# Optimization experiments

Hardware: AMD Instinct MI355X
Metric: run time of the kernel (lower is better)

The kernel has to match this reference:

```python
import jax, jax.numpy as jnp
import numpy as np

R_SAFE = 0.8

def setup_inputs() -> dict:
    key = jax.random.key(0)
    ks = jax.random.split(key, 12)
    B, F, H1, H21, H22, C = 524288, 10, 128, 32, 32, 2
    def lin(k, fan_in, fan_out):
        k1, k2 = jax.random.split(k)
        bound = 1.0 / np.sqrt(fan_in)
        W = jax.random.uniform(k1, (fan_out, fan_in), jnp.float32, -bound, bound)
        b = jax.random.uniform(k2, (fan_out,), jnp.float32, -bound, bound)
        return W, b
    W1, b1 = lin(ks[0], F, H1)
    W21, b21 = lin(ks[1], H1, H21)
    W22, b22 = lin(ks[2], H1, H22)
    W31, b31 = lin(ks[3], H21, C)
    W32, b32 = lin(ks[4], H22, 1)
    obs = jax.random.normal(ks[5], (B, F), jnp.float32)
    return {"obs": obs, "W1": W1, "b1": b1, "W21": W21, "b21": b21,
            "W22": W22, "b22": b22, "W31": W31, "b31": b31, "W32": W32, "b32": b32}

def _forward(obs, W1, b1, W21, b21, W22, b22, W31, b31, W32, b32):
    x = jax.nn.silu(obs @ W1.T + b1)          # [B, H1]
    x21 = jax.nn.silu(x @ W21.T + b21)        # [B, H21]
    x22 = jax.nn.silu(x @ W22.T + b22)        # [B, H22]
    unom = x21 @ W31.T + b31                  # [B, 2]
    alpha = 4.0 * jax.nn.sigmoid((x22 @ W32.T + b32)[:, 0])  # [B]
    rel_x, rel_y = obs[:, 6], obs[:, 7]
    v_hx, v_hy = obs[:, 8], obs[:, 9]
    barrier = rel_x**2 + rel_y**2 - R_SAFE**2
    lf = -2.0 * (rel_x * v_hx + rel_y * v_hy)
    # single inequality G u <= h with G = [-2 rel_x, -2 rel_y]
    G = jnp.stack([-2.0 * rel_x, -2.0 * rel_y], axis=1)      # [B, 2]
    h = lf + alpha * barrier                                  # [B]
    # QP: min ||u - unom||^2 s.t. G u <= h  ->  halfspace projection (exact KKT)
    gg = jnp.sum(G * G, axis=1)                               # [B]
    viol = jnp.sum(G * unom, axis=1) - h                      # [B]
    lam = jnp.where(gg > 0, jax.nn.relu(viol) / jnp.maximum(gg, 1e-12), 0.0)
    return unom - lam[:, None] * G

def reference(obs, W1, b1, W21, b21, W22, b22, W31, b31, W32, b32):
    return _forward(obs, W1, b1, W21, b21, W22, b22, W31, b31, W32, b32)
```

## Files before the change

kernel.cpp:

```cpp
#include <hip/hip_runtime.h>


typedef _Float16 half8 __attribute__((ext_vector_type(8)));
typedef float floatx4 __attribute__((ext_vector_type(4)));

#define TPB 256
#define NW  4

#define WS_FRAG 0
#define WS_B2Q  26624
#define WS_END  26880

__device__ __forceinline__ float fast_sigmoid(float z) {
    return __builtin_amdgcn_rcpf(1.0f + __expf(-z));
}

__device__ __forceinline__ void silu_pair(float z0, float z1,
                                          _Float16* o0, _Float16* o1) {
    float e0 = __expf(fminf(-z0, 30.0f));
    float e1 = __expf(fminf(-z1, 30.0f));
    float d0 = 1.0f + e0, d1 = 1.0f + e1;
    float r  = __builtin_amdgcn_rcpf(d0 * d1);
    *o0 = (_Float16)(z0 * d1 * r);
    *o1 = (_Float16)(z1 * d0 * r);
}

__global__ __launch_bounds__(256) void prep_kernel(
    const float* __restrict__ W1,  const float* __restrict__ b1,
    const float* __restrict__ W21, const float* __restrict__ b21,
    const float* __restrict__ W22, const float* __restrict__ b22,
    const float* __restrict__ W31, const float* __restrict__ b31,
    const float* __restrict__ W32, const float* __restrict__ b32,
    unsigned char* __restrict__ ws)
{
    const int tid  = blockIdx.x * 256 + threadIdx.x;
    const int lane = tid & 63;
    const int m    = lane & 15;
    const int q    = lane >> 4;

    if (tid < 26 * 64) {
        const int f = tid >> 6;
        float v[8];
        if (f < 8) {
            const float* wr = W1 + (f * 16 + m) * 10;
            #pragma unroll
            for (int j = 0; j < 8; ++j) {
                const int k = q * 8 + j;
                v[j] = (k < 10) ? wr[k] : (k == 10 ? b1[f * 16 + m] : 0.0f);
            }
        } else if (f < 24) {
            const int f2 = f - 8, nt2 = f2 >> 2, kt = f2 & 3;
            const int n2 = nt2 * 16 + m;
            const float* wr = (n2 < 32) ? (W21 + n2 * 128)
                                        : (W22 + (n2 - 32) * 128);
            #pragma unroll
            for (int j = 0; j < 8; ++j) {
                const int H = (2 * kt + (j >> 2)) * 16 + q * 4 + (j & 3);
                v[j] = wr[H];
            }
        } else {
            const int kt3 = f - 24;
            #pragma unroll
            for (int j = 0; j < 8; ++j) {
                const int H3 = (2 * kt3 + (j >> 2)) * 16 + q * 4 + (j & 3);
                float x = 0.0f;
                if (m == 0)      x = (H3 < 32)  ? W31[H3]       : 0.0f;
                else if (m == 1) x = (H3 < 32)  ? W31[32 + H3]  : 0.0f;
                else if (m == 2) x = (H3 >= 32) ? W32[H3 - 32]  : 0.0f;
                v[j] = x;
            }
        }
        half8 h;
        #pragma unroll
        for (int j = 0; j < 8; ++j) h[j] = (_Float16)v[j];
        ((half8*)(ws + WS_FRAG))[tid] = h;
    }
    if (tid < 16) {
        const int nt2 = tid >> 2, qq = tid & 3;
        float4 v;
        float* vp = (float*)&v;
        #pragma unroll
        for (int r = 0; r < 4; ++r) {
            const int n2 = nt2 * 16 + qq * 4 + r;
            vp[r] = (n2 < 32) ? b21[n2] : b22[n2 - 32];
        }
        ((float4*)(ws + WS_B2Q))[tid] = v;
    }
}

__global__ __launch_bounds__(TPB, 4) void barriernet_kernel(
    const float* __restrict__ obs,
    const unsigned char* __restrict__ ws,
    const float* __restrict__ b31, const float* __restrict__ b32,
    float* __restrict__ out, int B)
{
    __shared__ __align__(16) unsigned char lds[WS_END];

    const int tid  = threadIdx.x;
    const int wave = tid >> 6;
    const int lane = tid & 63;
    const int m    = lane & 15;
    const int q    = lane >> 4;

    {
        const float4* src = (const float4*)ws;
        float4* dst = (float4*)lds;
        for (int i = tid; i < WS_END / 16; i += TPB) dst[i] = src[i];
    }
    __syncthreads();

    const half8*  wl   = ((const half8*)lds) + lane;
    const float4* b2qt = (const float4*)(lds + WS_B2Q);

    const float bu0 = b31[0], bu1 = b31[1], bz3 = b32[0];

    const int tiles = (B + 15) >> 4;
    const int tbase = (blockIdx.x * NW + wave) * 2;

    const float* orow[2];
    half8 xf[2];
    int lrow0[2];
    #pragma unroll
    for (int p = 0; p < 2; ++p) {
        int tile = tbase + p;
        if (tile >= tiles) tile = tiles - 1;
        int lr = (tile << 4) + m;
        if (lr >= B) lr = B - 1;
        lrow0[p] = lr;
        orow[p] = obs + (size_t)lr * 10;

        float g0=0,g1=0,g2=0,g3=0,g4=0,g5=0,g6=0,g7=0;
        if (q == 0) {
            float2 p0 = *(const float2*)(orow[p] + 0);
            float2 p1 = *(const float2*)(orow[p] + 2);
            float2 p2 = *(const float2*)(orow[p] + 4);
            float2 p3 = *(const float2*)(orow[p] + 6);
            g0=p0.x; g1=p0.y; g2=p1.x; g3=p1.y;
            g4=p2.x; g5=p2.y; g6=p3.x; g7=p3.y;
        } else if (q == 1) {
            float2 pp = *(const float2*)(orow[p] + 8);
            g0=pp.x; g1=pp.y;
            g2=1.0f;
        }
        xf[p][0]=(_Float16)g0; xf[p][1]=(_Float16)g1;
        xf[p][2]=(_Float16)g2; xf[p][3]=(_Float16)g3;
        xf[p][4]=(_Float16)g4; xf[p][5]=(_Float16)g5;
        xf[p][6]=(_Float16)g6; xf[p][7]=(_Float16)g7;
    }

    half8 b2f[2][4];
    #pragma unroll
    for (int kt = 0; kt < 4; ++kt) {
        half8 w1a = wl[(2 * kt) * 64];
        half8 w1b = wl[(2 * kt + 1) * 64];
        #pragma unroll
        for (int p = 0; p < 2; ++p) {
            const floatx4 zz = {0.0f, 0.0f, 0.0f, 0.0f};
            floatx4 a0 = __builtin_amdgcn_mfma_f32_16x16x32_f16(
                             w1a, xf[p], zz, 0, 0, 0);
            floatx4 a1 = __builtin_amdgcn_mfma_f32_16x16x32_f16(
                             w1b, xf[p], zz, 0, 0, 0);
            half8 bf;
            #pragma unroll
            for (int jj = 0; jj < 4; ++jj) {
                _Float16 o0, o1;
                silu_pair(a0[jj], a1[jj], &o0, &o1);
                bf[jj] = o0; bf[jj + 4] = o1;
            }
            b2f[p][kt] = bf;
        }
    }

    floatx4 acc2[2][4];
    #pragma unroll
    for (int nt2 = 0; nt2 < 4; ++nt2) {
        float4 bi = b2qt[nt2 * 4 + q];
        floatx4 zi = {bi.x, bi.y, bi.z, bi.w};
        acc2[0][nt2] = zi;
        acc2[1][nt2] = zi;
        #pragma unroll
        for (int kt = 0; kt < 4; ++kt) {
            half8 wfr = wl[(8 + nt2 * 4 + kt) * 64];
            acc2[0][nt2] = __builtin_amdgcn_mfma_f32_16x16x32_f16(
                               wfr, b2f[0][kt], acc2[0][nt2], 0, 0, 0);
            acc2[1][nt2] = __builtin_amdgcn_mfma_f32_16x16x32_f16(
                               wfr, b2f[1][kt], acc2[1][nt2], 0, 0, 0);
        }
    }

    half8 b3f[2][2];
    #pragma unroll
    for (int kt3 = 0; kt3 < 2; ++kt3) {
        #pragma unroll
        for (int p = 0; p < 2; ++p) {
            half8 bf;
            #pragma unroll
            for (int jj = 0; jj < 4; ++jj) {
                _Float16 o0, o1;
                silu_pair(acc2[p][2 * kt3][jj], acc2[p][2 * kt3 + 1][jj],
                          &o0, &o1);
                bf[jj] = o0; bf[jj + 4] = o1;
            }
            b3f[p][kt3] = bf;
        }
    }

    half8 w3a = wl[24 * 64];
    half8 w3b = wl[25 * 64];
    #pragma unroll
    for (int p = 0; p < 2; ++p) {
        floatx4 d = {0.0f, 0.0f, 0.0f, 0.0f};
        d = __builtin_amdgcn_mfma_f32_16x16x32_f16(w3a, b3f[p][0], d, 0, 0, 0);
        d = __builtin_amdgcn_mfma_f32_16x16x32_f16(w3b, b3f[p][1], d, 0, 0, 0);
        if (q == 0) {
            const float u0  = d[0] + bu0;
            const float u1  = d[1] + bu1;
            const float z32 = d[2] + bz3;
            const float alpha = 4.0f * fast_sigmoid(z32);

            const float2 rxy = *(const float2*)(orow[p] + 6);
            const float2 vxy = *(const float2*)(orow[p] + 8);
            const float rx = rxy.x, ry = rxy.y, vx = vxy.x, vy = vxy.y;

            const float barrier = rx * rx + ry * ry - 0.64f;
            const float lf = -2.0f * (rx * vx + ry * vy);
            const float gx = -2.0f * rx, gy = -2.0f * ry;
            const float h  = lf + alpha * barrier;
            const float gg = gx * gx + gy * gy;
            const float viol = gx * u0 + gy * u1 - h;
            float lam = 0.0f;
            if (gg > 0.0f)
                lam = fmaxf(viol, 0.0f) *
                      __builtin_amdgcn_rcpf(fmaxf(gg, 1e-12f));

            float2 r;
            r.x = fmaf(-lam, gx, u0);
            r.y = fmaf(-lam, gy, u1);
            *(float2*)(out + (size_t)lrow0[p] * 2) = r;
        }
    }
}

extern "C" void kernel_launch(void* const* d_in, const int* in_sizes, int n_in,
                              void* d_out, int out_size, void* d_ws, size_t ws_size,
                              hipStream_t stream) {
    const float* obs = (const float*)d_in[0];
    const float* W1  = (const float*)d_in[1];
    const float* b1  = (const float*)d_in[2];
    const float* W21 = (const float*)d_in[3];
    const float* b21 = (const float*)d_in[4];
    const float* W22 = (const float*)d_in[5];
    const float* b22 = (const float*)d_in[6];
    const float* W31 = (const float*)d_in[7];
    const float* b31 = (const float*)d_in[8];
    const float* W32 = (const float*)d_in[9];
    const float* b32 = (const float*)d_in[10];

    unsigned char* ws = (unsigned char*)d_ws;

    prep_kernel<<<7, 256, 0, stream>>>(W1, b1, W21, b21, W22, b22,
                                       W31, b31, W32, b32, ws);

    const int B = in_sizes[0] / 10;
    const int tiles = (B + 15) / 16;
    const int pairs = (tiles + 1) / 2;
    const int grid  = (pairs + NW - 1) / NW;

    barriernet_kernel<<<grid, TPB, 0, stream>>>(obs, ws, b31, b32,
                                                (float*)d_out, B);
}
```

Before: 115.4 us.

## Fuse weight prep into main kernel and fold log2e scaling into weights

Removes the separate prep kernel launch: every block now builds the fp16 MFMA weight fragments directly in LDS from the raw fp32 weights. The weights and biases are pre-scaled by log2(e), and the last layer by ln2, so SiLU can use exp2 with fewer multiplies and an FMA-based shared reciprocal. The obs rx/ry values are also reused from registers instead of being reloaded. The cost is that every block repeats the weight gather and conversion from global memory, and accuracy may shift slightly in fp16.

```diff
diff --git a/kernel.cpp b/kernel.cpp
--- a/kernel.cpp
+++ b/kernel.cpp
@@ -15,83 +15,24 @@
     return __builtin_amdgcn_rcpf(1.0f + __expf(-z));
 }
 
-__device__ __forceinline__ void silu_pair(float z0, float z1,
-                                          _Float16* o0, _Float16* o1) {
-    float e0 = __expf(fminf(-z0, 30.0f));
-    float e1 = __expf(fminf(-z1, 30.0f));
-    float d0 = 1.0f + e0, d1 = 1.0f + e1;
-    float r  = __builtin_amdgcn_rcpf(d0 * d1);
-    *o0 = (_Float16)(z0 * d1 * r);
-    *o1 = (_Float16)(z1 * d0 * r);
-}
-
-__global__ __launch_bounds__(256) void prep_kernel(
+__device__ __forceinline__ void silu2s(float y0, float y1,
+                                       _Float16* o0, _Float16* o1) {
+    float e0 = exp2f(-y0);
+    float e1 = exp2f(-y1);
+    float d1 = 1.0f + e1;
+    float P  = __builtin_fmaf(e0, d1, d1);
+    float r  = __builtin_amdgcn_rcpf(P);
+    *o0 = (_Float16)((y0 * d1) * r);
+    *o1 = (_Float16)(__builtin_fmaf(y1, e0, y1) * r);
+}
+
+__global__ __launch_bounds__(TPB, 4) void barriernet_kernel(
+    const float* __restrict__ obs,
     const float* __restrict__ W1,  const float* __restrict__ b1,
     const float* __restrict__ W21, const float* __restrict__ b21,
     const float* __restrict__ W22, const float* __restrict__ b22,
     const float* __restrict__ W31, const float* __restrict__ b31,
     const float* __restrict__ W32, const float* __restrict__ b32,
-    unsigned char* __restrict__ ws)
-{
-    const int tid  = blockIdx.x * 256 + threadIdx.x;
-    const int lane = tid & 63;
-    const int m    = lane & 15;
-    const int q    = lane >> 4;
-
-    if (tid < 26 * 64) {
-        const int f = tid >> 6;
-        float v[8];
-        if (f < 8) {
-            const float* wr = W1 + (f * 16 + m) * 10;
-            #pragma unroll
-            for (int j = 0; j < 8; ++j) {
-                const int k = q * 8 + j;
-                v[j] = (k < 10) ? wr[k] : (k == 10 ? b1[f * 16 + m] : 0.0f);
-            }
-        } else if (f < 24) {
-            const int f2 = f - 8, nt2 = f2 >> 2, kt = f2 & 3;
-            const int n2 = nt2 * 16 + m;
-            const float* wr = (n2 < 32) ? (W21 + n2 * 128)
-                                        : (W22 + (n2 - 32) * 128);
-            #pragma unroll
-            for (int j = 0; j < 8; ++j) {
-                const int H = (2 * kt + (j >> 2)) * 16 + q * 4 + (j & 3);
-                v[j] = wr[H];
-            }
-        } else {
-            const int kt3 = f - 24;
-            #pragma unroll
-            for (int j = 0; j < 8; ++j) {
-                const int H3 = (2 * kt3 + (j >> 2)) * 16 + q * 4 + (j & 3);
-                float x = 0.0f;
-                if (m == 0)      x = (H3 < 32)  ? W31[H3]       : 0.0f;
-                else if (m == 1) x = (H3 < 32)  ? W31[32 + H3]  : 0.0f;
-                else if (m == 2) x = (H3 >= 32) ? W32[H3 - 32]  : 0.0f;
-                v[j] = x;
-            }
-        }
-        half8 h;
-        #pragma unroll
-        for (int j = 0; j < 8; ++j) h[j] = (_Float16)v[j];
-        ((half8*)(ws + WS_FRAG))[tid] = h;
-    }
-    if (tid < 16) {
-        const int nt2 = tid >> 2, qq = tid & 3;
-        float4 v;
-        float* vp = (float*)&v;
-        #pragma unroll
-        for (int r = 0; r < 4; ++r) {
-            const int n2 = nt2 * 16 + qq * 4 + r;
-            vp[r] = (n2 < 32) ? b21[n2] : b22[n2 - 32];
-        }
-        ((float4*)(ws + WS_B2Q))[tid] = v;
-    }
-}
-
-__global__ __launch_bounds__(TPB, 4) void barriernet_kernel(
-    const float* __restrict__ obs,
-    const unsigned char* __restrict__ ws,
-    const float* __restrict__ b31, const float* __restrict__ b32,
     float* __restrict__ out, int B)
 {
     __shared__ __align__(16) unsigned char lds[WS_END];
@@ -102,10 +43,79 @@
     const int m    = lane & 15;
     const int q    = lane >> 4;
 
-    {
-        const float4* src = (const float4*)ws;
-        float4* dst = (float4*)lds;
-        for (int i = tid; i < WS_END / 16; i += TPB) dst[i] = src[i];
+    const float C  = 1.44269504088896340736f;
+    const float CI = 0.69314718055994530942f;
+
+    for (int i = tid; i < 26 * 64; i += TPB) {
+        const int f  = i >> 6;
+        const int l  = i & 63;
+        const int mm = l & 15;
+        const int qq = l >> 4;
+        float v[8];
+        #pragma unroll
+        for (int j = 0; j < 8; ++j) v[j] = 0.0f;
+        if (f < 8) {
+            const float* wr = W1 + (f * 16 + mm) * 10;
+            if (qq == 0) {
+                float2 p0 = *(const float2*)(wr + 0);
+                float2 p1 = *(const float2*)(wr + 2);
+                float2 p2 = *(const float2*)(wr + 4);
+                float2 p3 = *(const float2*)(wr + 6);
+                v[0] = p0.x * C; v[1] = p0.y * C;
+                v[2] = p1.x * C; v[3] = p1.y * C;
+                v[4] = p2.x * C; v[5] = p2.y * C;
+                v[6] = p3.x * C; v[7] = p3.y * C;
+            } else if (qq == 1) {
+                float2 p4 = *(const float2*)(wr + 8);
+                v[0] = p4.x * C; v[1] = p4.y * C;
+                v[2] = b1[f * 16 + mm] * C;
+            }
+        } else if (f < 24) {
+            const int f2 = f - 8, nt2 = f2 >> 2, kt = f2 & 3;
+            const int n2 = nt2 * 16 + mm;
+            const float* wr = (n2 < 32) ? (W21 + n2 * 128)
+                                        : (W22 + (n2 - 32) * 128);
+            float4 a  = *(const float4*)(wr + (2 * kt) * 16 + qq * 4);
+            float4 bb = *(const float4*)(wr + (2 * kt + 1) * 16 + qq * 4);
+            v[0] = a.x;  v[1] = a.y;  v[2] = a.z;  v[3] = a.w;
+            v[4] = bb.x; v[5] = bb.y; v[6] = bb.z; v[7] = bb.w;
+        } else {
+            const int kt3 = f - 24;
+            float4 a = {0, 0, 0, 0}, bb = {0, 0, 0, 0};
+            if (kt3 == 0) {
+                if (mm == 0) {
+                    a  = *(const float4*)(W31 + qq * 4);
+                    bb = *(const float4*)(W31 + 16 + qq * 4);
+                } else if (mm == 1) {
+                    a  = *(const float4*)(W31 + 32 + qq * 4);
+                    bb = *(const float4*)(W31 + 48 + qq * 4);
+                }
+            } else {
+                if (mm == 2) {
+                    a  = *(const float4*)(W32 + qq * 4);
+                    bb = *(const float4*)(W32 + 16 + qq * 4);
+                }
+            }
+            v[0] = a.x * CI;  v[1] = a.y * CI;
+            v[2] = a.z * CI;  v[3] = a.w * CI;
+            v[4] = bb.x * CI; v[5] = bb.y * CI;
+            v[6] = bb.z * CI; v[7] = bb.w * CI;
+        }
+        half8 h;
+        #pragma unroll
+        for (int j = 0; j < 8; ++j) h[j] = (_Float16)v[j];
+        ((half8*)lds)[i] = h;
+    }
+    if (tid < 16) {
+        const int nt2 = tid >> 2, qq = tid & 3;
+        float4 v;
+        float* vp = (float*)&v;
+        #pragma unroll
+        for (int r = 0; r < 4; ++r) {
+            const int n2 = nt2 * 16 + qq * 4 + r;
+            vp[r] = ((n2 < 32) ? b21[n2] : b22[n2 - 32]) * C;
+        }
+        ((float4*)(lds + WS_B2Q))[tid] = v;
     }
     __syncthreads();
 
@@ -120,6 +130,7 @@
     const float* orow[2];
     half8 xf[2];
     int lrow0[2];
+    float rxs[2], rys[2];
     #pragma unroll
     for (int p = 0; p < 2; ++p) {
         int tile = tbase + p;
@@ -142,6 +153,7 @@
             g0=pp.x; g1=pp.y;
             g2=1.0f;
         }
+        rxs[p] = g6; rys[p] = g7;
         xf[p][0]=(_Float16)g0; xf[p][1]=(_Float16)g1;
         xf[p][2]=(_Float16)g2; xf[p][3]=(_Float16)g3;
         xf[p][4]=(_Float16)g4; xf[p][5]=(_Float16)g5;
@@ -164,7 +176,7 @@
             #pragma unroll
             for (int jj = 0; jj < 4; ++jj) {
                 _Float16 o0, o1;
-                silu_pair(a0[jj], a1[jj], &o0, &o1);
+                silu2s(a0[jj], a1[jj], &o0, &o1);
                 bf[jj] = o0; bf[jj + 4] = o1;
             }
             b2f[p][kt] = bf;
@@ -197,8 +209,8 @@
             #pragma unroll
             for (int jj = 0; jj < 4; ++jj) {
                 _Float16 o0, o1;
-                silu_pair(acc2[p][2 * kt3][jj], acc2[p][2 * kt3 + 1][jj],
-                          &o0, &o1);
+                silu2s(acc2[p][2 * kt3][jj], acc2[p][2 * kt3 + 1][jj],
+                       &o0, &o1);
                 bf[jj] = o0; bf[jj + 4] = o1;
             }
             b3f[p][kt3] = bf;
@@ -218,9 +230,9 @@
             const float z32 = d[2] + bz3;
             const float alpha = 4.0f * fast_sigmoid(z32);
 
-            const float2 rxy = *(const float2*)(orow[p] + 6);
+            const float rx = rxs[p], ry = rys[p];
             const float2 vxy = *(const float2*)(orow[p] + 8);
-            const float rx = rxy.x, ry = rxy.y, vx = vxy.x, vy = vxy.y;
+            const float vx = vxy.x, vy = vxy.y;
 
             const float barrier = rx * rx + ry * ry - 0.64f;
             const float lf = -2.0f * (rx * vx + ry * vy);
@@ -256,16 +268,14 @@
     const float* W32 = (const float*)d_in[9];
     const float* b32 = (const float*)d_in[10];
 
-    unsigned char* ws = (unsigned char*)d_ws;
-
-    prep_kernel<<<7, 256, 0, stream>>>(W1, b1, W21, b21, W22, b22,
-                                       W31, b31, W32, b32, ws);
+    (void)d_ws; (void)ws_size;
 
     const int B = in_sizes[0] / 10;
     const int tiles = (B + 15) / 16;
     const int pairs = (tiles + 1) / 2;
     const int grid  = (pairs + NW - 1) / NW;
 
-    barriernet_kernel<<<grid, TPB, 0, stream>>>(obs, ws, b31, b32,
-                                                (float*)d_out, B);
-}
+    barriernet_kernel<<<grid, TPB, 0, stream>>>(
+        obs, W1, b1, W21, b21, W22, b22, W31, b31, W32, b32,
+        (float*)d_out, B);
+}
```

New measurement: 129.6 us. +12.3%, slower.

## Use persistent grid-stride blocks and fold log2e scaling into weights for exp2 SiLU

Applied to the files above, without the earlier changes.

Layer-1 and layer-2 weights and biases are prescaled by log2(e) and the output weights by ln(2) in the prep kernel, so the SiLU can use exp2 directly with a fused single-reciprocal form. The main kernel becomes persistent: the grid is capped at 1280 blocks and each wave loops over tile pairs, so the LDS weight staging is paid once per block rather than once per pair. The occupancy hint rises from 4 to 5 blocks per SIMD, and rx/ry are kept in registers instead of being reloaded. Risks include tighter register limits from the higher occupancy hint and small precision changes from the scaled fp16 weights.

```diff
diff --git a/kernel.cpp b/kernel.cpp
--- a/kernel.cpp
+++ b/kernel.cpp
@@ -6,6 +6,7 @@
 
 #define TPB 256
 #define NW  4
+#define GRID 1280
 
 #define WS_FRAG 0
 #define WS_B2Q  26624
@@ -15,14 +16,15 @@
     return __builtin_amdgcn_rcpf(1.0f + __expf(-z));
 }
 
-__device__ __forceinline__ void silu_pair(float z0, float z1,
-                                          _Float16* o0, _Float16* o1) {
-    float e0 = __expf(fminf(-z0, 30.0f));
-    float e1 = __expf(fminf(-z1, 30.0f));
-    float d0 = 1.0f + e0, d1 = 1.0f + e1;
-    float r  = __builtin_amdgcn_rcpf(d0 * d1);
-    *o0 = (_Float16)(z0 * d1 * r);
-    *o1 = (_Float16)(z1 * d0 * r);
+__device__ __forceinline__ void silu2s(float y0, float y1,
+                                       _Float16* o0, _Float16* o1) {
+    float e0 = exp2f(-y0);
+    float e1 = exp2f(-y1);
+    float d1 = 1.0f + e1;
+    float P  = __builtin_fmaf(e0, d1, d1);
+    float r  = __builtin_amdgcn_rcpf(P);
+    *o0 = (_Float16)((y0 * d1) * r);
+    *o1 = (_Float16)(__builtin_fmaf(y1, e0, y1) * r);
 }
 
 __global__ __launch_bounds__(256) void prep_kernel(
@@ -33,6 +35,9 @@
     const float* __restrict__ W32, const float* __restrict__ b32,
     unsigned char* __restrict__ ws)
 {
+    const float C  = 1.44269504088896340736f;
+    const float CI = 0.69314718055994530942f;
+
     const int tid  = blockIdx.x * 256 + threadIdx.x;
     const int lane = tid & 63;
     const int m    = lane & 15;
@@ -46,7 +51,8 @@
             #pragma unroll
             for (int j = 0; j < 8; ++j) {
                 const int k = q * 8 + j;
-                v[j] = (k < 10) ? wr[k] : (k == 10 ? b1[f * 16 + m] : 0.0f);
+                float x = (k < 10) ? wr[k] : (k == 10 ? b1[f * 16 + m] : 0.0f);
+                v[j] = x * C;
             }
         } else if (f < 24) {
             const int f2 = f - 8, nt2 = f2 >> 2, kt = f2 & 3;
@@ -67,7 +73,7 @@
                 if (m == 0)      x = (H3 < 32)  ? W31[H3]       : 0.0f;
                 else if (m == 1) x = (H3 < 32)  ? W31[32 + H3]  : 0.0f;
                 else if (m == 2) x = (H3 >= 32) ? W32[H3 - 32]  : 0.0f;
-                v[j] = x;
+                v[j] = x * CI;
             }
         }
         half8 h;
@@ -82,13 +88,13 @@
         #pragma unroll
         for (int r = 0; r < 4; ++r) {
             const int n2 = nt2 * 16 + qq * 4 + r;
-            vp[r] = (n2 < 32) ? b21[n2] : b22[n2 - 32];
+            vp[r] = ((n2 < 32) ? b21[n2] : b22[n2 - 32]) * C;
         }
         ((float4*)(ws + WS_B2Q))[tid] = v;
     }
 }
 
-__global__ __launch_bounds__(TPB, 4) void barriernet_kernel(
+__global__ __launch_bounds__(TPB, 5) void barriernet_kernel(
     const float* __restrict__ obs,
     const unsigned char* __restrict__ ws,
     const float* __restrict__ b31, const float* __restrict__ b32,
@@ -114,129 +120,139 @@
 
     const float bu0 = b31[0], bu1 = b31[1], bz3 = b32[0];
 
-    const int tiles = (B + 15) >> 4;
-    const int tbase = (blockIdx.x * NW + wave) * 2;
-
-    const float* orow[2];
-    half8 xf[2];
-    int lrow0[2];
-    #pragma unroll
-    for (int p = 0; p < 2; ++p) {
-        int tile = tbase + p;
-        if (tile >= tiles) tile = tiles - 1;
-        int lr = (tile << 4) + m;
-        if (lr >= B) lr = B - 1;
-        lrow0[p] = lr;
-        orow[p] = obs + (size_t)lr * 10;
-
-        float g0=0,g1=0,g2=0,g3=0,g4=0,g5=0,g6=0,g7=0;
-        if (q == 0) {
-            float2 p0 = *(const float2*)(orow[p] + 0);
-            float2 p1 = *(const float2*)(orow[p] + 2);
-            float2 p2 = *(const float2*)(orow[p] + 4);
-            float2 p3 = *(const float2*)(orow[p] + 6);
-            g0=p0.x; g1=p0.y; g2=p1.x; g3=p1.y;
-            g4=p2.x; g5=p2.y; g6=p3.x; g7=p3.y;
-        } else if (q == 1) {
-            float2 pp = *(const float2*)(orow[p] + 8);
-            g0=pp.x; g1=pp.y;
-            g2=1.0f;
-        }
-        xf[p][0]=(_Float16)g0; xf[p][1]=(_Float16)g1;
-        xf[p][2]=(_Float16)g2; xf[p][3]=(_Float16)g3;
-        xf[p][4]=(_Float16)g4; xf[p][5]=(_Float16)g5;
-        xf[p][6]=(_Float16)g6; xf[p][7]=(_Float16)g7;
-    }
-
-    half8 b2f[2][4];
-    #pragma unroll
-    for (int kt = 0; kt < 4; ++kt) {
-        half8 w1a = wl[(2 * kt) * 64];
-        half8 w1b = wl[(2 * kt + 1) * 64];
+    const int tiles  = (B + 15) >> 4;
+    const int npairs = (tiles + 1) >> 1;
+    const int gwave  = blockIdx.x * NW + wave;
+    const int nwv    = gridDim.x * NW;
+
+    for (int pair = gwave; pair < npairs; pair += nwv) {
+        const int tbase = pair * 2;
+
+        const float* orow[2];
+        half8 xf[2];
+        int lrow0[2];
+        float rxs[2], rys[2];
         #pragma unroll
         for (int p = 0; p < 2; ++p) {
-            const floatx4 zz = {0.0f, 0.0f, 0.0f, 0.0f};
-            floatx4 a0 = __builtin_amdgcn_mfma_f32_16x16x32_f16(
-                             w1a, xf[p], zz, 0, 0, 0);
-            floatx4 a1 = __builtin_amdgcn_mfma_f32_16x16x32_f16(
-                             w1b, xf[p], zz, 0, 0, 0);
-            half8 bf;
-            #pragma unroll
-            for (int jj = 0; jj < 4; ++jj) {
-                _Float16 o0, o1;
-                silu_pair(a0[jj], a1[jj], &o0, &o1);
-                bf[jj] = o0; bf[jj + 4] = o1;
-            }
-            b2f[p][kt] = bf;
-        }
-    }
-
-    floatx4 acc2[2][4];
-    #pragma unroll
-    for (int nt2 = 0; nt2 < 4; ++nt2) {
-        float4 bi = b2qt[nt2 * 4 + q];
-        floatx4 zi = {bi.x, bi.y, bi.z, bi.w};
-        acc2[0][nt2] = zi;
-        acc2[1][nt2] = zi;
+            int tile = tbase + p;
+            if (tile >= tiles) tile = tiles - 1;
+            int lr = (tile << 4) + m;
+            if (lr >= B) lr = B - 1;
+            lrow0[p] = lr;
+            orow[p] = obs + (size_t)lr * 10;
+
+            float g0=0,g1=0,g2=0,g3=0,g4=0,g5=0,g6=0,g7=0;
+            if (q == 0) {
+                float2 p0 = *(const float2*)(orow[p] + 0);
+                float2 p1 = *(const float2*)(orow[p] + 2);
+                float2 p2 = *(const float2*)(orow[p] + 4);
+                float2 p3 = *(const float2*)(orow[p] + 6);
+                g0=p0.x; g1=p0.y; g2=p1.x; g3=p1.y;
+                g4=p2.x; g5=p2.y; g6=p3.x; g7=p3.y;
+            } else if (q == 1) {
+                float2 pp = *(const float2*)(orow[p] + 8);
+                g0=pp.x; g1=pp.y;
+                g2=1.0f;
+            }
+            rxs[p] = g6; rys[p] = g7;
+            xf[p][0]=(_Float16)g0; xf[p][1]=(_Float16)g1;
+            xf[p][2]=(_Float16)g2; xf[p][3]=(_Float16)g3;
+            xf[p][4]=(_Float16)g4; xf[p][5]=(_Float16)g5;
+            xf[p][6]=(_Float16)g6; xf[p][7]=(_Float16)g7;
+        }
+
+        half8 b2f[2][4];
         #pragma unroll
         for (int kt = 0; kt < 4; ++kt) {
-            half8 wfr = wl[(8 + nt2 * 4 + kt) * 64];
-            acc2[0][nt2] = __builtin_amdgcn_mfma_f32_16x16x32_f16(
-                               wfr, b2f[0][kt], acc2[0][nt2], 0, 0, 0);
-            acc2[1][nt2] = __builtin_amdgcn_mfma_f32_16x16x32_f16(
-                               wfr, b2f[1][kt], acc2[1][nt2], 0, 0, 0);
-        }
-    }
-
-    half8 b3f[2][2];
-    #pragma unroll
-    for (int kt3 = 0; kt3 < 2; ++kt3) {
+            half8 w1a = wl[(2 * kt) * 64];
+            half8 w1b = wl[(2 * kt + 1) * 64];
+            #pragma unroll
+            for (int p = 0; p < 2; ++p) {
+                const floatx4 zz = {0.0f, 0.0f, 0.0f, 0.0f};
+                floatx4 a0 = __builtin_amdgcn_mfma_f32_16x16x32_f16(
+                                 w1a, xf[p], zz, 0, 0, 0);
+                floatx4 a1 = __builtin_amdgcn_mfma_f32_16x16x32_f16(
+                                 w1b, xf[p], zz, 0, 0, 0);
+                half8 bf;
+                #pragma unroll
+                for (int jj = 0; jj < 4; ++jj) {
+                    _Float16 o0, o1;
+                    silu2s(a0[jj], a1[jj], &o0, &o1);
+                    bf[jj] = o0; bf[jj + 4] = o1;
+                }
+                b2f[p][kt] = bf;
+            }
+        }
+
+        floatx4 acc2[2][4];
+        #pragma unroll
+        for (int nt2 = 0; nt2 < 4; ++nt2) {
+            float4 bi = b2qt[nt2 * 4 + q];
+            floatx4 zi = {bi.x, bi.y, bi.z, bi.w};
+            acc2[0][nt2] = zi;
+            acc2[1][nt2] = zi;
+            #pragma unroll
+            for (int kt = 0; kt < 4; ++kt) {
+                half8 wfr = wl[(8 + nt2 * 4 + kt) * 64];
+                acc2[0][nt2] = __builtin_amdgcn_mfma_f32_16x16x32_f16(
+                                   wfr, b2f[0][kt], acc2[0][nt2], 0, 0, 0);
+                acc2[1][nt2] = __builtin_amdgcn_mfma_f32_16x16x32_f16(
+                                   wfr, b2f[1][kt], acc2[1][nt2], 0, 0, 0);
+            }
+        }
+
+        half8 b3f[2][2];
+        #pragma unroll
+        for (int kt3 = 0; kt3 < 2; ++kt3) {
+            #pragma unroll
+            for (int p = 0; p < 2; ++p) {
+                half8 bf;
+                #pragma unroll
+                for (int jj = 0; jj < 4; ++jj) {
+                    _Float16 o0, o1;
+                    silu2s(acc2[p][2 * kt3][jj], acc2[p][2 * kt3 + 1][jj],
+                           &o0, &o1);
+                    bf[jj] = o0; bf[jj + 4] = o1;
+                }
+                b3f[p][kt3] = bf;
+            }
+        }
+
+        half8 w3a = wl[24 * 64];
+        half8 w3b = wl[25 * 64];
         #pragma unroll
         for (int p = 0; p < 2; ++p) {
-            half8 bf;
-            #pragma unroll
-            for (int jj = 0; jj < 4; ++jj) {
-                _Float16 o0, o1;
-                silu_pair(acc2[p][2 * kt3][jj], acc2[p][2 * kt3 + 1][jj],
-                          &o0, &o1);
-                bf[jj] = o0; bf[jj + 4] = o1;
-            }
-            b3f[p][kt3] = bf;
-        }
-    }
-
-    half8 w3a = wl[24 * 64];
-    half8 w3b = wl[25 * 64];
-    #pragma unroll
-    for (int p = 0; p < 2; ++p) {
-        floatx4 d = {0.0f, 0.0f, 0.0f, 0.0f};
-        d = __builtin_amdgcn_mfma_f32_16x16x32_f16(w3a, b3f[p][0], d, 0, 0, 0);
-        d = __builtin_amdgcn_mfma_f32_16x16x32_f16(w3b, b3f[p][1], d, 0, 0, 0);
-        if (q == 0) {
-            const float u0  = d[0] + bu0;
-            const float u1  = d[1] + bu1;
-            const float z32 = d[2] + bz3;
-            const float alpha = 4.0f * fast_sigmoid(z32);
-
-            const float2 rxy = *(const float2*)(orow[p] + 6);
-            const float2 vxy = *(const float2*)(orow[p] + 8);
-            const float rx = rxy.x, ry = rxy.y, vx = vxy.x, vy = vxy.y;
-
-            const float barrier = rx * rx + ry * ry - 0.64f;
-            const float lf = -2.0f * (rx * vx + ry * vy);
-            const float gx = -2.0f * rx, gy = -2.0f * ry;
-            const float h  = lf + alpha * barrier;
-            const float gg = gx * gx + gy * gy;
-            const float viol = gx * u0 + gy * u1 - h;
-            float lam = 0.0f;
-            if (gg > 0.0f)
-                lam = fmaxf(viol, 0.0f) *
-                      __builtin_amdgcn_rcpf(fmaxf(gg, 1e-12f));
-
-            float2 r;
-            r.x = fmaf(-lam, gx, u0);
-            r.y = fmaf(-lam, gy, u1);
-            *(float2*)(out + (size_t)lrow0[p] * 2) = r;
+            floatx4 d = {0.0f, 0.0f, 0.0f, 0.0f};
+            d = __builtin_amdgcn_mfma_f32_16x16x32_f16(w3a, b3f[p][0], d,
+                                                       0, 0, 0);
+            d = __builtin_amdgcn_mfma_f32_16x16x32_f16(w3b, b3f[p][1], d,
+                                                       0, 0, 0);
+            if (q == 0) {
+                const float u0  = d[0] + bu0;
+                const float u1  = d[1] + bu1;
+                const float z32 = d[2] + bz3;
+                const float alpha = 4.0f * fast_sigmoid(z32);
+
+                const float rx = rxs[p], ry = rys[p];
+                const float2 vxy = *(const float2*)(orow[p] + 8);
+                const float vx = vxy.x, vy = vxy.y;
+
+                const float barrier = rx * rx + ry * ry - 0.64f;
+                const float lf = -2.0f * (rx * vx + ry * vy);
+                const float gx = -2.0f * rx, gy = -2.0f * ry;
+                const float h  = lf + alpha * barrier;
+                const float gg = gx * gx + gy * gy;
+                const float viol = gx * u0 + gy * u1 - h;
+                float lam = 0.0f;
+                if (gg > 0.0f)
+                    lam = fmaxf(viol, 0.0f) *
+                          __builtin_amdgcn_rcpf(fmaxf(gg, 1e-12f));
+
+                float2 r;
+                r.x = fmaf(-lam, gx, u0);
+                r.y = fmaf(-lam, gy, u1);
+                *(float2*)(out + (size_t)lrow0[p] * 2) = r;
+            }
         }
     }
 }
@@ -264,7 +280,8 @@
     const int B = in_sizes[0] / 10;
     const int tiles = (B + 15) / 16;
     const int pairs = (tiles + 1) / 2;
-    const int grid  = (pairs + NW - 1) / NW;
+    int grid = (pairs + NW - 1) / NW;
+    if (grid > GRID) grid = GRID;
 
     barriernet_kernel<<<grid, TPB, 0, stream>>>(obs, ws, b31, b32,
                                                 (float*)d_out, B);
```

Result: slower. 249.8 us (+116.5%).
